# Optimization experiments

Hardware: AMD Instinct MI355X
Metric: run time of the kernel (lower is better)

The kernel has to match this reference:

```python
import jax, jax.numpy as jnp
import numpy as np

ROPE_BASE = 10000.0


def _rope_cos_sin(seq_len, head_size, dtype):
    inv_freq = 1.0 / (ROPE_BASE ** (jnp.arange(0, head_size, 2, dtype=jnp.float32) / head_size))
    t = jnp.arange(seq_len, dtype=jnp.float32)
    freqs = jnp.outer(t, inv_freq)            # [S, D/2]
    emb = jnp.concatenate([freqs, freqs], axis=-1)  # [S, D]
    return jnp.cos(emb).astype(dtype), jnp.sin(emb).astype(dtype)


def _rotate_half(x):
    d = x.shape[-1] // 2
    return jnp.concatenate([-x[..., d:], x[..., :d]], axis=-1)


def setup_inputs() -> dict:
    key = jax.random.key(0)
    k1, k2, k3 = jax.random.split(key, 3)
    B, S, H, D = 2, 2048, 32, 128
    NUM_BLOCKS, BLOCK_SIZE = 512, 16
    q = jax.random.normal(k1, (B, S, H, D), dtype=jnp.float32)
    k = jax.random.normal(k2, (B, S, H, D), dtype=jnp.float32)
    v = jax.random.normal(k3, (B, S, H, D), dtype=jnp.float32)
    k_cache = jnp.zeros((NUM_BLOCKS, H, D, BLOCK_SIZE), dtype=jnp.float32)
    v_cache = jnp.zeros((NUM_BLOCKS, H, D, BLOCK_SIZE), dtype=jnp.float32)
    context_lengths = jnp.full((B,), S, dtype=jnp.int64)
    block_tables = jnp.arange(B * (S // BLOCK_SIZE), dtype=jnp.int64).reshape(B, S // BLOCK_SIZE)
    return {"q": q, "k": k, "v": v, "k_cache": k_cache, "v_cache": v_cache,
            "context_lengths": context_lengths, "block_tables": block_tables}


def reference(q, k, v, k_cache, v_cache, context_lengths, block_tables):
    # PagedAttention.pad_context_forward (prefill path, lengths == seq_len, block-aligned)
    B, S, H, D = q.shape
    block_size = k_cache.shape[-1]
    n_blk = S // block_size

    qt = q.transpose(0, 2, 1, 3)  # [B,H,S,D]
    kt = k.transpose(0, 2, 1, 3)
    vt = v.transpose(0, 2, 1, 3)

    cos, sin = _rope_cos_sin(S, D, q.dtype)  # [S,D], broadcast over B,H
    q_rot = qt * cos + _rotate_half(qt) * sin
    k_rot = kt * cos + _rotate_half(kt) * sin

    # copy_to_cache (prefill): scatter rotated keys and raw values into paged caches
    def to_blocks(x_bshd):  # [B,S,H,D] -> [B*n_blk, H, D, block_size]
        xb = x_bshd.reshape(B, n_blk, block_size, H, D)
        return xb.transpose(0, 1, 3, 4, 2).reshape(B * n_blk, H, D, block_size)

    k_cache_new = k_cache.at[block_tables.reshape(-1)].set(to_blocks(k_rot.transpose(0, 2, 1, 3)))
    v_cache_new = v_cache.at[block_tables.reshape(-1)].set(to_blocks(v))

    # dense causal attention, fp32 softmax
    scores = jnp.einsum('bhqd,bhkd->bhqk', q_rot, k_rot) / jnp.sqrt(jnp.asarray(D, q.dtype))
    causal = jnp.tril(jnp.ones((S, S), dtype=bool))
    scores = scores + jnp.where(causal, jnp.asarray(0.0, q.dtype), jnp.finfo(q.dtype).min)
    weights = jax.nn.softmax(scores.astype(jnp.float32), axis=-1).astype(q.dtype)
    out = jnp.einsum('bhqk,bhkd->bhqd', weights, vt)  # note: original uses un-rotated v
    attn_output = out.transpose(0, 2, 1, 3).reshape(B, S, H * D)
    return attn_output, k_cache_new, v_cache_new
```

## Files before the change

kernel.cpp:

```cpp
#include <hip/hip_runtime.h>
#include <math.h>

#define B 2
#define S 2048
#define H 32
#define D 128
#define BS 16
#define NBLK (S / BS)
#define NT 256

#define FREQ_C 0.20762050593045953f
#define SCALE 0.08838834764831845f

typedef __attribute__((ext_vector_type(8))) short short8;
typedef __attribute__((ext_vector_type(4))) float floatx4;

__device__ __forceinline__ unsigned short f2bf(float x) {
  return (unsigned short)((__float_as_uint(x) + 0x8000u) >> 16);
}
__device__ __forceinline__ unsigned packbf(float lo, float hi) {
  unsigned ua = __float_as_uint(lo) + 0x8000u;
  unsigned ub = __float_as_uint(hi) + 0x8000u;
  return (ub & 0xFFFF0000u) | (ua >> 16);
}

__device__ __forceinline__ void gload_lds16(const void* g, void* l) {
  __builtin_amdgcn_global_load_lds(
      (const __attribute__((address_space(1))) void*)g,
      (__attribute__((address_space(3))) void*)l, 16, 0, 0);
}

__global__ __launch_bounds__(256) void build_tbl(float* __restrict__ tbl) {
  int i = blockIdx.x * 256 + threadIdx.x;
  int s = i >> 6, j = i & 63;
  float fr = exp2f(-(float)j * FREQ_C);
  float sn, cs;
  sincosf((float)s * fr, &sn, &cs);
  tbl[s * 128 + j] = cs;
  tbl[s * 128 + 64 + j] = sn;
}

__global__ __launch_bounds__(NT) void rope_scatter2(
    const float* __restrict__ k, const float* __restrict__ v,
    const int* __restrict__ block_tables,
    float* __restrict__ k_out, float* __restrict__ v_out,
    unsigned short* __restrict__ kbf, unsigned short* __restrict__ vtb,
    const float* __restrict__ tbl) {
  int idx = blockIdx.x;
  int h = idx % H;
  int m = idx / H;
  int b = m / NBLK;
  int sblk = m % NBLK;
  int phys = block_tables[m];

  __shared__ float Ks[BS][D + 4];
  __shared__ float Vs[BS][D + 4];
  __shared__ float Kr[BS][D + 4];
  __shared__ float Tc[BS][D + 4];
  int tid = threadIdx.x;

  const size_t in_base = (((size_t)b * S + (size_t)sblk * BS) * H + h) * D;
  const float* trow = tbl + (size_t)sblk * BS * 128;
  for (int p = 0; p < (BS * D) / NT; ++p) {
    int f = p * NT + tid;
    int row = f >> 7, d = f & 127;
    size_t g = in_base + (size_t)row * (H * D) + d;
    Ks[row][d] = k[g];
    Vs[row][d] = v[g];
    Tc[row][d] = trow[row * 128 + d];
  }
  __syncthreads();

  size_t out_base = ((size_t)phys * H + h) * (D * BS);
  for (int p = 0; p < (BS * D) / NT; ++p) {
    int f = p * NT + tid;
    int d = f >> 4, t = f & 15;
    float cs = Tc[t][d & 63];
    float sn = Tc[t][64 + (d & 63)];
    float x = Ks[t][d];
    float xr = (d < 64) ? -Ks[t][d + 64] : Ks[t][d - 64];
    float r = x * cs + xr * sn;
    k_out[out_base + f] = r;
    v_out[out_base + f] = Vs[t][d];
    Kr[t][d] = r;
  }
  __syncthreads();

  const int kt = sblk >> 2, cb = sblk & 3;
  unsigned* kb32 = (unsigned*)kbf +
      (((size_t)(b * H + h) * (S / 64) + kt) * 64 + (size_t)cb * 16) * (D / 2);
  for (int p = 0; p < (BS * D / 2) / NT; ++p) {
    int e = p * NT + tid;
    int t = e >> 6, dp = e & 63;
    float2 kr2 = *(const float2*)&Kr[t][2 * dp];
    kb32[t * 64 + (dp ^ ((t & 7) << 2))] = packbf(kr2.x, kr2.y);
  }
  unsigned* vb32 = (unsigned*)vtb +
      ((size_t)(b * H + h) * (S / 64) + kt) * (D * 64 / 2);
  for (int p = 0; p < (BS * D / 2) / NT; ++p) {
    int e = p * NT + tid;
    int d = e >> 3, tp = e & 7;
    vb32[d * 32 + ((cb * 8 + tp) ^ ((d & 7) << 2))] =
        packbf(Vs[2 * tp][d], Vs[2 * tp + 1][d]);
  }
}

__global__ __launch_bounds__(NT, 2) void attn_mfma3(
    const float* __restrict__ q, const unsigned short* __restrict__ kbf,
    const unsigned short* __restrict__ vtb, const float* __restrict__ tbl,
    float* __restrict__ out) {
  __shared__ unsigned short Kls[2][64 * 128];
  __shared__ unsigned short Vls[2][128 * 64];
  __shared__ unsigned short Pb[4][16][72];

  const int qt = (S / 64 - 1) - (int)blockIdx.x;
  const int bh = blockIdx.y;
  const int b = bh >> 5, h = bh & 31;
  const int tid = threadIdx.x;
  const int lane = tid & 63, w = tid >> 6;
  const int n = lane & 15, quad = lane >> 4;

  short8 qf[4];
  {
    const int sq = qt * 64 + w * 16 + n;
    const float* qr = q + (((size_t)b * S + sq) * H + h) * D;
    const float* tr = tbl + (size_t)sq * 128;
#pragma unroll
    for (int ks = 0; ks < 4; ++ks) {
      int d0 = ks * 32 + quad * 8;
      float x[8], p[8], cs[8], sn[8];
      *(float4*)&x[0] = *(const float4*)(qr + d0);
      *(float4*)&x[4] = *(const float4*)(qr + d0 + 4);
      *(float4*)&p[0] = *(const float4*)(qr + (d0 ^ 64));
      *(float4*)&p[4] = *(const float4*)(qr + (d0 ^ 64) + 4);
      int dm = d0 & 63;
      *(float4*)&cs[0] = *(const float4*)(tr + dm);
      *(float4*)&cs[4] = *(const float4*)(tr + dm + 4);
      *(float4*)&sn[0] = *(const float4*)(tr + 64 + dm);
      *(float4*)&sn[4] = *(const float4*)(tr + 64 + dm + 4);
      unsigned short tmp[8];
#pragma unroll
      for (int i = 0; i < 8; ++i) {
        float r = (d0 < 64) ? (x[i] * cs[i] - p[i] * sn[i])
                            : (x[i] * cs[i] + p[i] * sn[i]);
        tmp[i] = f2bf(r * SCALE);
      }
      qf[ks] = *(short8*)tmp;
    }
  }

  const floatx4 zero = {0.f, 0.f, 0.f, 0.f};
  floatx4 Ot[8];
#pragma unroll
  for (int dt = 0; dt < 8; ++dt) Ot[dt] = zero;
  float m_run[4], l_run[4];
#pragma unroll
  for (int r = 0; r < 4; ++r) {
    m_run[r] = -INFINITY;
    l_run[r] = 0.f;
  }

  const char* Kg = (const char*)(kbf + (size_t)(b * H + h) * (S / 64) * (64 * D));
  const char* Vg = (const char*)(vtb + (size_t)(b * H + h) * (S / 64) * (D * 64));
  const int soff = w * 4096 + (lane << 4);

  auto STAGE = [&](int buf, int t2) {
    const char* ks = Kg + (size_t)t2 * 16384 + soff;
    const char* vs = Vg + (size_t)t2 * 16384 + soff;
    char* kd = (char*)&Kls[buf][0] + w * 4096;
    char* vd = (char*)&Vls[buf][0] + w * 4096;
#pragma unroll
    for (int i = 0; i < 4; ++i) {
      gload_lds16(ks + i * 1024, kd + i * 1024);
      gload_lds16(vs + i * 1024, vd + i * 1024);
    }
  };

  int cur = 0;
  STAGE(0, 0);
  __syncthreads();

  const int sw = (n & 7) << 4;

  for (int kt = 0; kt <= qt; ++kt) {
    if (kt < qt) STAGE(cur ^ 1, kt + 1);

    const char* Kb = (const char*)&Kls[cur][0];
    const char* Vb = (const char*)&Vls[cur][0];

    floatx4 acc[4];
#pragma unroll
    for (int ct = 0; ct < 4; ++ct) {
      floatx4 a = zero;
#pragma unroll
      for (int ks = 0; ks < 4; ++ks) {
        short8 kf = *(const short8*)(
            Kb + (((ct * 16 + n) * 256 + ks * 64 + quad * 16) ^ sw));
        a = __builtin_amdgcn_mfma_f32_16x16x32_bf16(qf[ks], kf, a, 0, 0, 0);
      }
      acc[ct] = a;
    }

    if (kt == qt) {
#pragma unroll
      for (int ct = 0; ct < 4; ++ct)
#pragma unroll
        for (int r = 0; r < 4; ++r)
          if (ct * 16 + n > w * 16 + quad * 4 + r) acc[ct][r] = -INFINITY;
    }

    float mnew[4], alpha[4], rs[4];
#pragma unroll
    for (int r = 0; r < 4; ++r) {
      float v = fmaxf(fmaxf(acc[0][r], acc[1][r]), fmaxf(acc[2][r], acc[3][r]));
      v = fmaxf(v, __shfl_xor(v, 1));
      v = fmaxf(v, __shfl_xor(v, 2));
      v = fmaxf(v, __shfl_xor(v, 4));
      v = fmaxf(v, __shfl_xor(v, 8));
      mnew[r] = fmaxf(m_run[r], v);
      alpha[r] = __expf(m_run[r] - mnew[r]);
      m_run[r] = mnew[r];
    }
    float pv[4][4];
#pragma unroll
    for (int r = 0; r < 4; ++r) rs[r] = 0.f;
#pragma unroll
    for (int ct = 0; ct < 4; ++ct)
#pragma unroll
      for (int r = 0; r < 4; ++r) {
        float e = __expf(acc[ct][r] - mnew[r]);
        pv[ct][r] = e;
        rs[r] += e;
      }
#pragma unroll
    for (int r = 0; r < 4; ++r) {
      float s = rs[r];
      s += __shfl_xor(s, 1);
      s += __shfl_xor(s, 2);
      s += __shfl_xor(s, 4);
      s += __shfl_xor(s, 8);
      l_run[r] = l_run[r] * alpha[r] + s;
    }

#pragma unroll
    for (int dt = 0; dt < 8; ++dt)
#pragma unroll
      for (int r = 0; r < 4; ++r) Ot[dt][r] *= alpha[r];

#pragma unroll
    for (int ct = 0; ct < 4; ++ct)
#pragma unroll
      for (int r = 0; r < 4; ++r)
        Pb[w][quad * 4 + r][ct * 16 + n] = f2bf(pv[ct][r]);
    __builtin_amdgcn_wave_barrier();

    short8 pf0 = *(const short8*)&Pb[w][n][quad * 8];
    short8 pf1 = *(const short8*)&Pb[w][n][32 + quad * 8];
#pragma unroll
    for (int dt = 0; dt < 8; ++dt) {
      short8 vf0 = *(const short8*)(
          Vb + (((dt * 16 + n) * 128 + quad * 16) ^ sw));
      short8 vf1 = *(const short8*)(
          Vb + (((dt * 16 + n) * 128 + 64 + quad * 16) ^ sw));
      Ot[dt] = __builtin_amdgcn_mfma_f32_16x16x32_bf16(pf0, vf0, Ot[dt], 0, 0, 0);
      Ot[dt] = __builtin_amdgcn_mfma_f32_16x16x32_bf16(pf1, vf1, Ot[dt], 0, 0, 0);
    }
    __syncthreads();
    cur ^= 1;
  }

  float linv[4];
#pragma unroll
  for (int r = 0; r < 4; ++r) linv[r] = 1.f / l_run[r];
#pragma unroll
  for (int r = 0; r < 4; ++r) {
    int row = qt * 64 + w * 16 + quad * 4 + r;
    float* orow = out + ((size_t)(b * S + row) * H + h) * D + n;
#pragma unroll
    for (int dt = 0; dt < 8; ++dt) orow[dt * 16] = Ot[dt][r] * linv[r];
  }
}

__global__ __launch_bounds__(NT) void rope_scatter(
    const float* __restrict__ k, const float* __restrict__ v,
    const int* __restrict__ block_tables,
    float* __restrict__ k_out, float* __restrict__ v_out) {
  int idx = blockIdx.x;
  int h = idx % H;
  int m = idx / H;
  int b = m / NBLK;
  int sblk = m % NBLK;
  int phys = block_tables[m];

  __shared__ float Ks[BS][D + 4];
  __shared__ float Vs[BS][D + 4];
  int tid = threadIdx.x;

  const size_t in_base = (((size_t)b * S + (size_t)sblk * BS) * H + h) * D;
  for (int p = 0; p < (BS * D) / NT; ++p) {
    int f = p * NT + tid;
    int row = f >> 7, d = f & 127;
    size_t g = in_base + (size_t)row * (H * D) + d;
    Ks[row][d] = k[g];
    Vs[row][d] = v[g];
  }
  __syncthreads();

  size_t out_base = ((size_t)phys * H + h) * (D * BS);
  for (int p = 0; p < (BS * D) / NT; ++p) {
    int f = p * NT + tid;
    int d = f >> 4, t = f & 15;
    int s = sblk * BS + t;
    float fr = exp2f(-(float)(d & 63) * FREQ_C);
    float sn, cs;
    sincosf((float)s * fr, &sn, &cs);
    float x = Ks[t][d];
    float xr = (d < 64) ? -Ks[t][d + 64] : Ks[t][d - 64];
    k_out[out_base + f] = x * cs + xr * sn;
    v_out[out_base + f] = Vs[t][d];
  }
}

__global__ __launch_bounds__(NT, 3) void attn_mfma(
    const float* __restrict__ q, const float* __restrict__ kc,
    const float* __restrict__ vc, const int* __restrict__ bt,
    float* __restrict__ out) {
  __shared__ unsigned short Ks[64][136];
  __shared__ unsigned short Vt[128][72];
  __shared__ unsigned short Pb[4][16][72];

  const int qt = (S / 64 - 1) - (int)blockIdx.x;
  const int bh = blockIdx.y;
  const int b = bh >> 5, h = bh & 31;
  const int tid = threadIdx.x;
  const int lane = tid & 63, w = tid >> 6;
  const int n = lane & 15, quad = lane >> 4;

  short8 qf[4];
  {
    const int sq = qt * 64 + w * 16 + n;
    const float* qr = q + (((size_t)b * S + sq) * H + h) * D;
#pragma unroll
    for (int ks = 0; ks < 4; ++ks) {
      int d0 = ks * 32 + quad * 8;
      float x[8], p[8];
      *(float4*)&x[0] = *(const float4*)(qr + d0);
      *(float4*)&x[4] = *(const float4*)(qr + d0 + 4);
      *(float4*)&p[0] = *(const float4*)(qr + (d0 ^ 64));
      *(float4*)&p[4] = *(const float4*)(qr + (d0 ^ 64) + 4);
      unsigned short tmp[8];
#pragma unroll
      for (int i = 0; i < 8; ++i) {
        int d = d0 + i;
        float fr = exp2f(-(float)(d & 63) * FREQ_C);
        float sn, cs;
        __sincosf((float)sq * fr, &sn, &cs);
        float r = (d < 64) ? (x[i] * cs - p[i] * sn) : (x[i] * cs + p[i] * sn);
        tmp[i] = f2bf(r * SCALE);
      }
      qf[ks] = *(short8*)tmp;
    }
  }

  const floatx4 zero = {0.f, 0.f, 0.f, 0.f};
  floatx4 Ot[8];
#pragma unroll
  for (int dt = 0; dt < 8; ++dt) Ot[dt] = zero;
  float m_run[4], l_run[4];
#pragma unroll
  for (int r = 0; r < 4; ++r) {
    m_run[r] = -INFINITY;
    l_run[r] = 0.f;
  }

  for (int kt = 0; kt <= qt; ++kt) {
    int m4 = b * NBLK + kt * 4;
#pragma unroll
    for (int cb = 0; cb < 4; ++cb) {
      const size_t cbase = ((size_t)bt[m4 + cb] * H + h) * (D * BS);
      const float* ks_src = kc + cbase;
      const float* vs_src = vc + cbase;
#pragma unroll
      for (int it = 0; it < 4; ++it) {
        int rem = it * NT + tid;
        int dp = rem >> 4, t = rem & 15;
        float a0 = ks_src[(2 * dp) * BS + t];
        float a1 = ks_src[(2 * dp + 1) * BS + t];
        *(unsigned*)&Ks[cb * 16 + t][2 * dp] = packbf(a0, a1);
      }
#pragma unroll
      for (int it = 0; it < 4; ++it) {
        int rem = it * NT + tid;
        int d = rem >> 3, tp = rem & 7;
        float2 vv = *(const float2*)(vs_src + d * BS + tp * 2);
        *(unsigned*)&Vt[d][cb * 16 + tp * 2] = packbf(vv.x, vv.y);
      }
    }
    __syncthreads();

    floatx4 acc[4];
#pragma unroll
    for (int ct = 0; ct < 4; ++ct) {
      floatx4 a = zero;
#pragma unroll
      for (int ks = 0; ks < 4; ++ks) {
        short8 kf = *(const short8*)&Ks[ct * 16 + n][ks * 32 + quad * 8];
        a = __builtin_amdgcn_mfma_f32_16x16x32_bf16(qf[ks], kf, a, 0, 0, 0);
      }
      acc[ct] = a;
    }

    if (kt == qt) {
#pragma unroll
      for (int ct = 0; ct < 4; ++ct)
#pragma unroll
        for (int r = 0; r < 4; ++r)
          if (ct * 16 + n > w * 16 + quad * 4 + r) acc[ct][r] = -INFINITY;
    }

    float mnew[4], alpha[4], rs[4];
#pragma unroll
    for (int r = 0; r < 4; ++r) {
      float v = fmaxf(fmaxf(acc[0][r], acc[1][r]), fmaxf(acc[2][r], acc[3][r]));
      v = fmaxf(v, __shfl_xor(v, 1));
      v = fmaxf(v, __shfl_xor(v, 2));
      v = fmaxf(v, __shfl_xor(v, 4));
      v = fmaxf(v, __shfl_xor(v, 8));
      mnew[r] = fmaxf(m_run[r], v);
      alpha[r] = __expf(m_run[r] - mnew[r]);
      m_run[r] = mnew[r];
    }
    float pv[4][4];
#pragma unroll
    for (int r = 0; r < 4; ++r) rs[r] = 0.f;
#pragma unroll
    for (int ct = 0; ct < 4; ++ct)
#pragma unroll
      for (int r = 0; r < 4; ++r) {
        float e = __expf(acc[ct][r] - mnew[r]);
        pv[ct][r] = e;
        rs[r] += e;
      }
#pragma unroll
    for (int r = 0; r < 4; ++r) {
      float s = rs[r];
      s += __shfl_xor(s, 1);
      s += __shfl_xor(s, 2);
      s += __shfl_xor(s, 4);
      s += __shfl_xor(s, 8);
      l_run[r] = l_run[r] * alpha[r] + s;
    }

#pragma unroll
    for (int dt = 0; dt < 8; ++dt)
#pragma unroll
      for (int r = 0; r < 4; ++r) Ot[dt][r] *= alpha[r];

#pragma unroll
    for (int ct = 0; ct < 4; ++ct)
#pragma unroll
      for (int r = 0; r < 4; ++r)
        Pb[w][quad * 4 + r][ct * 16 + n] = f2bf(pv[ct][r]);
    __builtin_amdgcn_wave_barrier();

    short8 pf0 = *(const short8*)&Pb[w][n][quad * 8];
    short8 pf1 = *(const short8*)&Pb[w][n][32 + quad * 8];
#pragma unroll
    for (int dt = 0; dt < 8; ++dt) {
      short8 vf0 = *(const short8*)&Vt[dt * 16 + n][quad * 8];
      short8 vf1 = *(const short8*)&Vt[dt * 16 + n][32 + quad * 8];
      Ot[dt] = __builtin_amdgcn_mfma_f32_16x16x32_bf16(pf0, vf0, Ot[dt], 0, 0, 0);
      Ot[dt] = __builtin_amdgcn_mfma_f32_16x16x32_bf16(pf1, vf1, Ot[dt], 0, 0, 0);
    }
    __syncthreads();
  }

  float linv[4];
#pragma unroll
  for (int r = 0; r < 4; ++r) linv[r] = 1.f / l_run[r];
#pragma unroll
  for (int r = 0; r < 4; ++r) {
    int row = qt * 64 + w * 16 + quad * 4 + r;
    float* orow = out + ((size_t)(b * S + row) * H + h) * D + n;
#pragma unroll
    for (int dt = 0; dt < 8; ++dt) orow[dt * 16] = Ot[dt][r] * linv[r];
  }
}

extern "C" void kernel_launch(void* const* d_in, const int* in_sizes, int n_in,
                              void* d_out, int out_size, void* d_ws,
                              size_t ws_size, hipStream_t stream) {
  const float* q = (const float*)d_in[0];
  const float* k = (const float*)d_in[1];
  const float* v = (const float*)d_in[2];
  const int* block_tables = (const int*)d_in[6];

  float* out_attn = (float*)d_out;
  float* out_kc = out_attn + (size_t)B * S * H * D;
  float* out_vc = out_kc + (size_t)512 * H * D * BS;

  hipMemsetAsync(out_kc, 0, (size_t)512 * H * D * BS * sizeof(float), stream);
  hipMemsetAsync(out_vc, 0, (size_t)512 * H * D * BS * sizeof(float), stream);

  const size_t kbf_elems = (size_t)B * H * S * D;
  const size_t need = kbf_elems * 2 * 2 + (size_t)S * 128 * sizeof(float);

  if (d_ws != nullptr && ws_size >= need) {
    unsigned short* kbf = (unsigned short*)d_ws;
    unsigned short* vtb = kbf + kbf_elems;
    float* tbl = (float*)(vtb + kbf_elems);

    build_tbl<<<(S * 64) / 256, 256, 0, stream>>>(tbl);
    rope_scatter2<<<B * NBLK * H, NT, 0, stream>>>(k, v, block_tables, out_kc,
                                                   out_vc, kbf, vtb, tbl);
    dim3 grid(S / 64, B * H);
    attn_mfma3<<<grid, NT, 0, stream>>>(q, kbf, vtb, tbl, out_attn);
  } else {
    rope_scatter<<<B * NBLK * H, NT, 0, stream>>>(k, v, block_tables, out_kc,
                                                  out_vc);
    dim3 grid(S / 64, B * H);
    attn_mfma<<<grid, NT, 0, stream>>>(q, out_kc, out_vc, block_tables,
                                       out_attn);
  }
}
```

Before: 888.7 us.

## Use 128-row query tiles with interleaved KV buffer and skip memset of mapped blocks

The attention kernel now processes 128 query rows per 512-thread workgroup (8 waves), so each staged K/V tile is shared by twice as many waves. K and V are packed into one contiguous interleaved buffer so a single staging pass loads both. The workgroup order is also remapped across heads and query tiles, and the P scratch buffer in shared memory gets an XOR swizzle to cut bank conflicts. The full-cache memsets are replaced by a bitmap kernel that zeroes only cache blocks not covered by the block table, which avoids writing the scattered blocks twice. In exchange, causal-edge waves sit idle on tiles past their diagonal, and there are two extra small kernel launches.

```diff
diff --git a/kernel.cpp b/kernel.cpp
--- a/kernel.cpp
+++ b/kernel.cpp
@@ -40,12 +40,35 @@
   tbl[s * 128 + 64 + j] = sn;
 }
 
+__global__ __launch_bounds__(512) void map_blocks(
+    const int* __restrict__ bt, int* __restrict__ bitmap) {
+  int t = threadIdx.x;
+  bitmap[t] = 0;
+  __syncthreads();
+  if (t < B * NBLK) bitmap[bt[t]] = 1;
+}
+
+__global__ __launch_bounds__(256) void zero_unmapped(
+    const int* __restrict__ bitmap, float* __restrict__ k_out,
+    float* __restrict__ v_out) {
+  int p = blockIdx.x;
+  if (bitmap[p]) return;
+  size_t base = (size_t)p * (H * D * BS) + (size_t)blockIdx.y * 8192;
+  float4 z = {0.f, 0.f, 0.f, 0.f};
+  float4* kd = (float4*)(k_out + base);
+  float4* vd = (float4*)(v_out + base);
+#pragma unroll
+  for (int i = 0; i < 8; ++i) {
+    kd[i * 256 + threadIdx.x] = z;
+    vd[i * 256 + threadIdx.x] = z;
+  }
+}
+
 __global__ __launch_bounds__(NT) void rope_scatter2(
     const float* __restrict__ k, const float* __restrict__ v,
     const int* __restrict__ block_tables,
     float* __restrict__ k_out, float* __restrict__ v_out,
-    unsigned short* __restrict__ kbf, unsigned short* __restrict__ vtb,
-    const float* __restrict__ tbl) {
+    unsigned short* __restrict__ kvb, const float* __restrict__ tbl) {
   int idx = blockIdx.x;
   int h = idx % H;
   int m = idx / H;
@@ -87,16 +110,15 @@
   __syncthreads();
 
   const int kt = sblk >> 2, cb = sblk & 3;
-  unsigned* kb32 = (unsigned*)kbf +
-      (((size_t)(b * H + h) * (S / 64) + kt) * 64 + (size_t)cb * 16) * (D / 2);
+  const size_t tb = ((size_t)(b * H + h) * (S / 64) + kt) * 16384;
+  unsigned* kb32 = (unsigned*)(kvb + tb) + (size_t)cb * 16 * 64;
   for (int p = 0; p < (BS * D / 2) / NT; ++p) {
     int e = p * NT + tid;
     int t = e >> 6, dp = e & 63;
     float2 kr2 = *(const float2*)&Kr[t][2 * dp];
     kb32[t * 64 + (dp ^ ((t & 7) << 2))] = packbf(kr2.x, kr2.y);
   }
-  unsigned* vb32 = (unsigned*)vtb +
-      ((size_t)(b * H + h) * (S / 64) + kt) * (D * 64 / 2);
+  unsigned* vb32 = (unsigned*)(kvb + tb + 8192);
   for (int p = 0; p < (BS * D / 2) / NT; ++p) {
     int e = p * NT + tid;
     int d = e >> 3, tp = e & 7;
@@ -105,16 +127,16 @@
   }
 }
 
-__global__ __launch_bounds__(NT, 2) void attn_mfma3(
-    const float* __restrict__ q, const unsigned short* __restrict__ kbf,
-    const unsigned short* __restrict__ vtb, const float* __restrict__ tbl,
-    float* __restrict__ out) {
-  __shared__ unsigned short Kls[2][64 * 128];
-  __shared__ unsigned short Vls[2][128 * 64];
-  __shared__ unsigned short Pb[4][16][72];
-
-  const int qt = (S / 64 - 1) - (int)blockIdx.x;
-  const int bh = blockIdx.y;
+__global__ __launch_bounds__(512, 4) void attn_mfma4(
+    const float* __restrict__ q, const unsigned short* __restrict__ kvb,
+    const float* __restrict__ tbl, float* __restrict__ out) {
+  __shared__ unsigned short KV[2][16384];
+  __shared__ unsigned short Pb[8][16][64];
+
+  const int wgid = blockIdx.x;
+  const int slot = wgid >> 3;
+  const int bh = (slot >> 4) * 8 + (wgid & 7);
+  const int qt = 15 - (slot & 15);
   const int b = bh >> 5, h = bh & 31;
   const int tid = threadIdx.x;
   const int lane = tid & 63, w = tid >> 6;
@@ -122,7 +144,7 @@
 
   short8 qf[4];
   {
-    const int sq = qt * 64 + w * 16 + n;
+    const int sq = qt * 128 + w * 16 + n;
     const float* qr = q + (((size_t)b * S + sq) * H + h) * D;
     const float* tr = tbl + (size_t)sq * 128;
 #pragma unroll
@@ -160,110 +182,114 @@
     l_run[r] = 0.f;
   }
 
-  const char* Kg = (const char*)(kbf + (size_t)(b * H + h) * (S / 64) * (64 * D));
-  const char* Vg = (const char*)(vtb + (size_t)(b * H + h) * (S / 64) * (D * 64));
-  const int soff = w * 4096 + (lane << 4);
+  const unsigned short* KVg = kvb + (size_t)bh * (S / 64) * 16384;
 
   auto STAGE = [&](int buf, int t2) {
-    const char* ks = Kg + (size_t)t2 * 16384 + soff;
-    const char* vs = Vg + (size_t)t2 * 16384 + soff;
-    char* kd = (char*)&Kls[buf][0] + w * 4096;
-    char* vd = (char*)&Vls[buf][0] + w * 4096;
-#pragma unroll
-    for (int i = 0; i < 4; ++i) {
-      gload_lds16(ks + i * 1024, kd + i * 1024);
-      gload_lds16(vs + i * 1024, vd + i * 1024);
-    }
+    const char* src =
+        (const char*)(KVg + (size_t)t2 * 16384) + w * 4096 + (lane << 4);
+    char* dst = (char*)&KV[buf][0] + w * 4096;
+#pragma unroll
+    for (int i = 0; i < 4; ++i) gload_lds16(src + i * 1024, dst + i * 1024);
   };
 
+  const int last = 2 * qt + 1;
   int cur = 0;
   STAGE(0, 0);
   __syncthreads();
 
   const int sw = (n & 7) << 4;
 
-  for (int kt = 0; kt <= qt; ++kt) {
-    if (kt < qt) STAGE(cur ^ 1, kt + 1);
-
-    const char* Kb = (const char*)&Kls[cur][0];
-    const char* Vb = (const char*)&Vls[cur][0];
-
-    floatx4 acc[4];
-#pragma unroll
-    for (int ct = 0; ct < 4; ++ct) {
-      floatx4 a = zero;
-#pragma unroll
-      for (int ks = 0; ks < 4; ++ks) {
-        short8 kf = *(const short8*)(
-            Kb + (((ct * 16 + n) * 256 + ks * 64 + quad * 16) ^ sw));
-        a = __builtin_amdgcn_mfma_f32_16x16x32_bf16(qf[ks], kf, a, 0, 0, 0);
-      }
-      acc[ct] = a;
-    }
-
-    if (kt == qt) {
+  for (int kt = 0; kt <= last; ++kt) {
+    if (kt < last) STAGE(cur ^ 1, kt + 1);
+
+    const bool active = (kt * 64 <= qt * 128 + w * 16 + 15);
+    if (active) {
+      const char* Kb = (const char*)&KV[cur][0];
+      const char* Vb = Kb + 16384;
+
+      floatx4 acc[4];
+#pragma unroll
+      for (int ct = 0; ct < 4; ++ct) {
+        floatx4 a = zero;
+#pragma unroll
+        for (int ks = 0; ks < 4; ++ks) {
+          short8 kf = *(const short8*)(
+              Kb + (((ct * 16 + n) * 256 + ks * 64 + quad * 16) ^ sw));
+          a = __builtin_amdgcn_mfma_f32_16x16x32_bf16(qf[ks], kf, a, 0, 0, 0);
+        }
+        acc[ct] = a;
+      }
+
+      if (kt >= 2 * qt) {
+        int lim = w * 16 + quad * 4 - (kt - 2 * qt) * 64;
+#pragma unroll
+        for (int ct = 0; ct < 4; ++ct)
+#pragma unroll
+          for (int r = 0; r < 4; ++r)
+            if (ct * 16 + n > lim + r) acc[ct][r] = -INFINITY;
+      }
+
+      float mnew[4], alpha[4], rs[4];
+#pragma unroll
+      for (int r = 0; r < 4; ++r) {
+        float v =
+            fmaxf(fmaxf(acc[0][r], acc[1][r]), fmaxf(acc[2][r], acc[3][r]));
+        v = fmaxf(v, __shfl_xor(v, 1));
+        v = fmaxf(v, __shfl_xor(v, 2));
+        v = fmaxf(v, __shfl_xor(v, 4));
+        v = fmaxf(v, __shfl_xor(v, 8));
+        mnew[r] = fmaxf(m_run[r], v);
+        alpha[r] = __expf(m_run[r] - mnew[r]);
+        m_run[r] = mnew[r];
+      }
+      float pv[4][4];
+#pragma unroll
+      for (int r = 0; r < 4; ++r) rs[r] = 0.f;
 #pragma unroll
       for (int ct = 0; ct < 4; ++ct)
 #pragma unroll
-        for (int r = 0; r < 4; ++r)
-          if (ct * 16 + n > w * 16 + quad * 4 + r) acc[ct][r] = -INFINITY;
-    }
-
-    float mnew[4], alpha[4], rs[4];
-#pragma unroll
-    for (int r = 0; r < 4; ++r) {
-      float v = fmaxf(fmaxf(acc[0][r], acc[1][r]), fmaxf(acc[2][r], acc[3][r]));
-      v = fmaxf(v, __shfl_xor(v, 1));
-      v = fmaxf(v, __shfl_xor(v, 2));
-      v = fmaxf(v, __shfl_xor(v, 4));
-      v = fmaxf(v, __shfl_xor(v, 8));
-      mnew[r] = fmaxf(m_run[r], v);
-      alpha[r] = __expf(m_run[r] - mnew[r]);
-      m_run[r] = mnew[r];
-    }
-    float pv[4][4];
-#pragma unroll
-    for (int r = 0; r < 4; ++r) rs[r] = 0.f;
-#pragma unroll
-    for (int ct = 0; ct < 4; ++ct)
+        for (int r = 0; r < 4; ++r) {
+          float e = __expf(acc[ct][r] - mnew[r]);
+          pv[ct][r] = e;
+          rs[r] += e;
+        }
 #pragma unroll
       for (int r = 0; r < 4; ++r) {
-        float e = __expf(acc[ct][r] - mnew[r]);
-        pv[ct][r] = e;
-        rs[r] += e;
-      }
-#pragma unroll
-    for (int r = 0; r < 4; ++r) {
-      float s = rs[r];
-      s += __shfl_xor(s, 1);
-      s += __shfl_xor(s, 2);
-      s += __shfl_xor(s, 4);
-      s += __shfl_xor(s, 8);
-      l_run[r] = l_run[r] * alpha[r] + s;
-    }
-
-#pragma unroll
-    for (int dt = 0; dt < 8; ++dt)
-#pragma unroll
-      for (int r = 0; r < 4; ++r) Ot[dt][r] *= alpha[r];
-
-#pragma unroll
-    for (int ct = 0; ct < 4; ++ct)
-#pragma unroll
-      for (int r = 0; r < 4; ++r)
-        Pb[w][quad * 4 + r][ct * 16 + n] = f2bf(pv[ct][r]);
-    __builtin_amdgcn_wave_barrier();
-
-    short8 pf0 = *(const short8*)&Pb[w][n][quad * 8];
-    short8 pf1 = *(const short8*)&Pb[w][n][32 + quad * 8];
-#pragma unroll
-    for (int dt = 0; dt < 8; ++dt) {
-      short8 vf0 = *(const short8*)(
-          Vb + (((dt * 16 + n) * 128 + quad * 16) ^ sw));
-      short8 vf1 = *(const short8*)(
-          Vb + (((dt * 16 + n) * 128 + 64 + quad * 16) ^ sw));
-      Ot[dt] = __builtin_amdgcn_mfma_f32_16x16x32_bf16(pf0, vf0, Ot[dt], 0, 0, 0);
-      Ot[dt] = __builtin_amdgcn_mfma_f32_16x16x32_bf16(pf1, vf1, Ot[dt], 0, 0, 0);
+        float s = rs[r];
+        s += __shfl_xor(s, 1);
+        s += __shfl_xor(s, 2);
+        s += __shfl_xor(s, 4);
+        s += __shfl_xor(s, 8);
+        l_run[r] = l_run[r] * alpha[r] + s;
+      }
+
+#pragma unroll
+      for (int dt = 0; dt < 8; ++dt)
+#pragma unroll
+        for (int r = 0; r < 4; ++r) Ot[dt][r] *= alpha[r];
+
+#pragma unroll
+      for (int ct = 0; ct < 4; ++ct)
+#pragma unroll
+        for (int r = 0; r < 4; ++r) {
+          int row = quad * 4 + r;
+          Pb[w][row][(ct * 16 + n) ^ ((row & 7) << 3)] = f2bf(pv[ct][r]);
+        }
+      __builtin_amdgcn_wave_barrier();
+
+      short8 pf0 = *(const short8*)&Pb[w][n][(quad * 8) ^ ((n & 7) << 3)];
+      short8 pf1 = *(const short8*)&Pb[w][n][(32 + quad * 8) ^ ((n & 7) << 3)];
+#pragma unroll
+      for (int dt = 0; dt < 8; ++dt) {
+        short8 vf0 = *(const short8*)(
+            Vb + (((dt * 16 + n) * 128 + quad * 16) ^ sw));
+        short8 vf1 = *(const short8*)(
+            Vb + (((dt * 16 + n) * 128 + 64 + quad * 16) ^ sw));
+        Ot[dt] =
+            __builtin_amdgcn_mfma_f32_16x16x32_bf16(pf0, vf0, Ot[dt], 0, 0, 0);
+        Ot[dt] =
+            __builtin_amdgcn_mfma_f32_16x16x32_bf16(pf1, vf1, Ot[dt], 0, 0, 0);
+      }
     }
     __syncthreads();
     cur ^= 1;
@@ -274,7 +300,7 @@
   for (int r = 0; r < 4; ++r) linv[r] = 1.f / l_run[r];
 #pragma unroll
   for (int r = 0; r < 4; ++r) {
-    int row = qt * 64 + w * 16 + quad * 4 + r;
+    int row = qt * 128 + w * 16 + quad * 4 + r;
     float* orow = out + ((size_t)(b * S + row) * H + h) * D + n;
 #pragma unroll
     for (int dt = 0; dt < 8; ++dt) orow[dt * 16] = Ot[dt][r] * linv[r];
@@ -499,23 +525,25 @@
   float* out_kc = out_attn + (size_t)B * S * H * D;
   float* out_vc = out_kc + (size_t)512 * H * D * BS;
 
-  hipMemsetAsync(out_kc, 0, (size_t)512 * H * D * BS * sizeof(float), stream);
-  hipMemsetAsync(out_vc, 0, (size_t)512 * H * D * BS * sizeof(float), stream);
-
-  const size_t kbf_elems = (size_t)B * H * S * D;
-  const size_t need = kbf_elems * 2 * 2 + (size_t)S * 128 * sizeof(float);
+  const size_t kvb_shorts = (size_t)B * H * (S / 64) * 16384;
+  const size_t tbl_floats = (size_t)S * 128;
+  const size_t need = kvb_shorts * 2 + tbl_floats * 4 + 2048;
 
   if (d_ws != nullptr && ws_size >= need) {
-    unsigned short* kbf = (unsigned short*)d_ws;
-    unsigned short* vtb = kbf + kbf_elems;
-    float* tbl = (float*)(vtb + kbf_elems);
+    unsigned short* kvb = (unsigned short*)d_ws;
+    float* tbl = (float*)(kvb + kvb_shorts);
+    int* bitmap = (int*)(tbl + tbl_floats);
+
+    map_blocks<<<1, 512, 0, stream>>>(block_tables, bitmap);
+    zero_unmapped<<<dim3(512, 8), 256, 0, stream>>>(bitmap, out_kc, out_vc);
 
     build_tbl<<<(S * 64) / 256, 256, 0, stream>>>(tbl);
     rope_scatter2<<<B * NBLK * H, NT, 0, stream>>>(k, v, block_tables, out_kc,
-                                                   out_vc, kbf, vtb, tbl);
-    dim3 grid(S / 64, B * H);
-    attn_mfma3<<<grid, NT, 0, stream>>>(q, kbf, vtb, tbl, out_attn);
+                                                   out_vc, kvb, tbl);
+    attn_mfma4<<<(S / 128) * B * H, 512, 0, stream>>>(q, kvb, tbl, out_attn);
   } else {
+    hipMemsetAsync(out_kc, 0, (size_t)512 * H * D * BS * sizeof(float), stream);
+    hipMemsetAsync(out_vc, 0, (size_t)512 * H * D * BS * sizeof(float), stream);
     rope_scatter<<<B * NBLK * H, NT, 0, stream>>>(k, v, block_tables, out_kc,
                                                   out_vc);
     dim3 grid(S / 64, B * H);
```

After: 854.3 us. 3.9% less time.
